# Optimization experiments

Hardware: AMD Instinct MI355X
Metric: run time of the kernel (lower is better)

The kernel has to match this reference:

```python
import jax, jax.numpy as jnp
import numpy as np
from jax import lax

B, T, U, F, K = 128, 4096, 128, 32, 31
WIN = 7  # attention_win_size
NEG = jnp.float32(-2.0**32 + 1)


def setup_inputs() -> dict:
    key = jax.random.key(0)
    ks = jax.random.split(key, 8)
    return {
        "query": jax.random.normal(ks[0], (B, U), jnp.float32),
        "state": jax.random.uniform(ks[1], (B, T), jnp.float32),
        "memory": jax.random.normal(ks[2], (B, T, U), jnp.float32) * 0.1,
        "conv_w": jax.random.normal(ks[3], (K, 1, F), jnp.float32) * 0.1,
        "conv_b": jnp.zeros((F,), jnp.float32),
        "loc_w": jax.random.normal(ks[4], (F, U), jnp.float32) * 0.1,
        "v_a": jax.random.normal(ks[5], (U,), jnp.float32) * 0.1,
        "b_a": jnp.zeros((U,), jnp.float32),
        "prev_max_attentions": jax.random.randint(ks[6], (B,), 0, T, jnp.int32),
    }


def reference(query, state, memory, conv_w, conv_b, loc_w, v_a, b_a, prev_max_attentions):
    # processed_query: [B, 1, U]
    processed_query = query[:, None, :]
    # location features: Conv1D 'same' over [B, T, 1] -> [B, T, F]
    loc_feat = lax.conv_general_dilated(
        state[:, :, None], conv_w, window_strides=(1,), padding="SAME",
        dimension_numbers=("NWC", "WIO", "NWC")) + conv_b
    # processed_location_features: [B, T, U]
    proc_loc = jnp.einsum("btf,fu->btu", loc_feat, loc_w)
    # Bahdanau location-sensitive score -> energy [B, T]
    energy = jnp.sum(v_a * jnp.tanh(memory + processed_query + proc_loc + b_a), axis=2)
    # synthesis constraint, 'window' type
    Tx = energy.shape[-1]
    idx = jnp.arange(Tx)
    key_masks = idx[None, :] < (prev_max_attentions - (WIN // 2 + (WIN % 2 != 0)))[:, None]
    reverse_masks = (idx[None, :] < (Tx - WIN // 2 - prev_max_attentions)[:, None])[:, ::-1]
    masks = key_masks | reverse_masks
    energy = jnp.where(masks, NEG, energy)
    alignments = jax.nn.softmax(energy, axis=-1)
    max_attentions = jnp.argmax(alignments, axis=-1).astype(jnp.int32)
    next_state = alignments + state  # cumulate_weights=True
    return alignments, next_state, max_attentions
```

## Files before the change

### kernel.cpp

```cpp
#include <hip/hip_runtime.h>
#include <math.h>

namespace {

constexpr int B_ = 128;
constexpr int T_ = 4096;
constexpr int U_ = 128;
constexpr int F_ = 32;
constexpr int K_ = 31;
constexpr int WIN_ = 7;
constexpr int SLICES = 4;
constexpr int SLICE_W = T_ / SLICES;
constexpr int NTHREADS = 256;

__global__ __launch_bounds__(NTHREADS) void lsa_kernel(
    const float* __restrict__ query,
    const float* __restrict__ state,
    const float* __restrict__ memory,
    const float* __restrict__ conv_w,
    const float* __restrict__ conv_b,
    const float* __restrict__ loc_w,
    const float* __restrict__ v_a,
    const float* __restrict__ b_a,
    const int*   __restrict__ prev,
    float* __restrict__ out_align,
    float* __restrict__ out_state,
    float* __restrict__ out_maxattn)
{
    const int b     = blockIdx.y;
    const int slice = blockIdx.x;
    const int tid   = threadIdx.x;

    const int pm = prev[b];
    const int lo = max(0, pm - 4);
    const int hi = min(T_ - 1, pm + 2);
    const int w  = hi - lo + 1;

    __shared__ float s_loc[WIN_][F_];
    __shared__ float s_energy[WIN_];
    __shared__ float s_align[WIN_];
    __shared__ float s_red[4];
    __shared__ int   s_amax;

    if (tid < w * F_) {
        const int j = tid / F_;
        const int f = tid % F_;
        const int t = lo + j;
        float acc = conv_b[f];
        #pragma unroll
        for (int k = 0; k < K_; ++k) {
            const int src = t + k - (K_ / 2);
            const float sv = (src >= 0 && src < T_) ? state[(size_t)b * T_ + src] : 0.f;
            acc += sv * conv_w[k * F_ + f];
        }
        s_loc[j][f] = acc;
    }
    __syncthreads();

    const int u    = tid & (U_ - 1);
    const int grp  = tid >> 7;
    const int wave = tid >> 6;
    const float q  = query[b * U_ + u];
    const float va = v_a[u];
    const float ba = b_a[u];

    for (int j0 = 0; j0 < WIN_; j0 += 2) {
        const int j = j0 + grp;
        float e = 0.f;
        if (j < w) {
            float pl = 0.f;
            #pragma unroll
            for (int f = 0; f < F_; ++f)
                pl += s_loc[j][f] * loc_w[f * U_ + u];
            const int t = lo + j;
            const float m = memory[((size_t)b * T_ + t) * U_ + u];
            e = va * tanhf(m + q + pl + ba);
        }
        #pragma unroll
        for (int off = 32; off > 0; off >>= 1)
            e += __shfl_down(e, off);
        if ((tid & 63) == 0) s_red[wave] = e;
        __syncthreads();
        if (tid == 0   && j0 < w)     s_energy[j0]     = s_red[0] + s_red[1];
        if (tid == 128 && j0 + 1 < w) s_energy[j0 + 1] = s_red[2] + s_red[3];
        __syncthreads();
    }

    if (tid == 0) {
        float mx = s_energy[0];
        for (int j = 1; j < w; ++j) mx = fmaxf(mx, s_energy[j]);
        float a[WIN_];
        float sum = 0.f;
        for (int j = 0; j < w; ++j) { a[j] = expf(s_energy[j] - mx); sum += a[j]; }
        for (int j = 0; j < w; ++j) { a[j] = a[j] / sum; s_align[j] = a[j]; }
        float best = -1.f; int bj = 0;
        for (int j = 0; j < w; ++j)
            if (a[j] > best) { best = a[j]; bj = j; }
        s_amax = lo + bj;
    }
    __syncthreads();

    const size_t row  = (size_t)b * T_;
    const int    base = slice * SLICE_W;
    const float4* st4 = reinterpret_cast<const float4*>(state + row + base);
    float4* oa4 = reinterpret_cast<float4*>(out_align + row + base);
    float4* os4 = reinterpret_cast<float4*>(out_state + row + base);

    {
        const int i  = tid;
        const int t0 = base + i * 4;
        const float4 sv = st4[i];
        float4 av;
        av.x = (t0 + 0 >= lo && t0 + 0 <= hi) ? s_align[t0 + 0 - lo] : 0.f;
        av.y = (t0 + 1 >= lo && t0 + 1 <= hi) ? s_align[t0 + 1 - lo] : 0.f;
        av.z = (t0 + 2 >= lo && t0 + 2 <= hi) ? s_align[t0 + 2 - lo] : 0.f;
        av.w = (t0 + 3 >= lo && t0 + 3 <= hi) ? s_align[t0 + 3 - lo] : 0.f;
        float4 ns;
        ns.x = sv.x + av.x;
        ns.y = sv.y + av.y;
        ns.z = sv.z + av.z;
        ns.w = sv.w + av.w;
        oa4[i] = av;
        os4[i] = ns;
    }

    if (slice == 0 && tid == 0)
        out_maxattn[b] = (float)s_amax;
}

}

extern "C" void kernel_launch(void* const* d_in, const int* in_sizes, int n_in,
                              void* d_out, int out_size, void* d_ws, size_t ws_size,
                              hipStream_t stream) {
    const float* query  = (const float*)d_in[0];
    const float* state  = (const float*)d_in[1];
    const float* memory = (const float*)d_in[2];
    const float* conv_w = (const float*)d_in[3];
    const float* conv_b = (const float*)d_in[4];
    const float* loc_w  = (const float*)d_in[5];
    const float* v_a    = (const float*)d_in[6];
    const float* b_a    = (const float*)d_in[7];
    const int*   prev   = (const int*)d_in[8];

    float* out = (float*)d_out;
    float* out_align   = out;
    float* out_state   = out + (size_t)B_ * T_;
    float* out_maxattn = out + (size_t)2 * B_ * T_;

    dim3 grid(SLICES, B_);
    lsa_kernel<<<grid, NTHREADS, 0, stream>>>(
        query, state, memory, conv_w, conv_b, loc_w, v_a, b_a, prev,
        out_align, out_state, out_maxattn);
}
```

Baseline: 15.01 us.

## Skip window computation in slices not touching it and vectorize energy per warp

```diff
diff --git a/kernel.cpp b/kernel.cpp
--- a/kernel.cpp
+++ b/kernel.cpp
@@ -30,6 +30,7 @@
     const int b     = blockIdx.y;
     const int slice = blockIdx.x;
     const int tid   = threadIdx.x;
+    const int base  = slice * SLICE_W;
 
     const int pm = prev[b];
     const int lo = max(0, pm - 4);
@@ -39,77 +40,83 @@
     __shared__ float s_loc[WIN_][F_];
     __shared__ float s_energy[WIN_];
     __shared__ float s_align[WIN_];
-    __shared__ float s_red[4];
     __shared__ int   s_amax;
 
-    if (tid < w * F_) {
-        const int j = tid / F_;
-        const int f = tid % F_;
-        const int t = lo + j;
-        float acc = conv_b[f];
-        #pragma unroll
-        for (int k = 0; k < K_; ++k) {
-            const int src = t + k - (K_ / 2);
-            const float sv = (src >= 0 && src < T_) ? state[(size_t)b * T_ + src] : 0.f;
-            acc += sv * conv_w[k * F_ + f];
+    const size_t row = (size_t)b * T_;
+    const float4 sv  = reinterpret_cast<const float4*>(state + row + base)[tid];
+
+    const bool has_pm     = (pm >= base) && (pm < base + SLICE_W);
+    const bool has_window = (base <= hi) && (base + SLICE_W > lo);
+
+    if (has_window || has_pm) {
+        const int j    = tid >> 5;
+        const int lane = tid & 31;
+
+        float4 mv = make_float4(0.f, 0.f, 0.f, 0.f);
+        if (j < w) {
+            const int t = lo + j;
+            mv = reinterpret_cast<const float4*>(memory + (row + t) * U_)[lane];
         }
-        s_loc[j][f] = acc;
-    }
-    __syncthreads();
+        const float4 q4  = reinterpret_cast<const float4*>(query + (size_t)b * U_)[lane];
+        const float4 va4 = reinterpret_cast<const float4*>(v_a)[lane];
+        const float4 ba4 = reinterpret_cast<const float4*>(b_a)[lane];
 
-    const int u    = tid & (U_ - 1);
-    const int grp  = tid >> 7;
-    const int wave = tid >> 6;
-    const float q  = query[b * U_ + u];
-    const float va = v_a[u];
-    const float ba = b_a[u];
+        if (tid < w * F_) {
+            const int cj = tid / F_;
+            const int f  = tid % F_;
+            const int t  = lo + cj;
+            float acc = conv_b[f];
+            #pragma unroll
+            for (int k = 0; k < K_; ++k) {
+                const int src = t + k - (K_ / 2);
+                const float svv = (src >= 0 && src < T_) ? state[row + src] : 0.f;
+                acc += svv * conv_w[k * F_ + f];
+            }
+            s_loc[cj][f] = acc;
+        }
+        __syncthreads();
 
-    for (int j0 = 0; j0 < WIN_; j0 += 2) {
-        const int j = j0 + grp;
         float e = 0.f;
         if (j < w) {
-            float pl = 0.f;
+            float4 pl = make_float4(0.f, 0.f, 0.f, 0.f);
             #pragma unroll
-            for (int f = 0; f < F_; ++f)
-                pl += s_loc[j][f] * loc_w[f * U_ + u];
-            const int t = lo + j;
-            const float m = memory[((size_t)b * T_ + t) * U_ + u];
-            e = va * tanhf(m + q + pl + ba);
+            for (int f = 0; f < F_; ++f) {
+                const float lf = s_loc[j][f];
+                const float4 lw = reinterpret_cast<const float4*>(loc_w + f * U_)[lane];
+                pl.x += lf * lw.x; pl.y += lf * lw.y;
+                pl.z += lf * lw.z; pl.w += lf * lw.w;
+            }
+            e  = va4.x * tanhf(mv.x + q4.x + pl.x + ba4.x);
+            e += va4.y * tanhf(mv.y + q4.y + pl.y + ba4.y);
+            e += va4.z * tanhf(mv.z + q4.z + pl.z + ba4.z);
+            e += va4.w * tanhf(mv.w + q4.w + pl.w + ba4.w);
         }
         #pragma unroll
-        for (int off = 32; off > 0; off >>= 1)
-            e += __shfl_down(e, off);
-        if ((tid & 63) == 0) s_red[wave] = e;
+        for (int off = 16; off > 0; off >>= 1)
+            e += __shfl_xor(e, off);
+        if (lane == 0 && j < w) s_energy[j] = e;
         __syncthreads();
-        if (tid == 0   && j0 < w)     s_energy[j0]     = s_red[0] + s_red[1];
-        if (tid == 128 && j0 + 1 < w) s_energy[j0 + 1] = s_red[2] + s_red[3];
+
+        if (tid == 0) {
+            float mx = s_energy[0];
+            for (int jj = 1; jj < w; ++jj) mx = fmaxf(mx, s_energy[jj]);
+            float a[WIN_];
+            float sum = 0.f;
+            for (int jj = 0; jj < w; ++jj) { a[jj] = expf(s_energy[jj] - mx); sum += a[jj]; }
+            const float inv = 1.f / sum;
+            float best = -1.f; int bj = 0;
+            for (int jj = 0; jj < w; ++jj) {
+                const float av = a[jj] * inv;
+                s_align[jj] = av;
+                if (av > best) { best = av; bj = jj; }
+            }
+            s_amax = lo + bj;
+        }
         __syncthreads();
     }
 
-    if (tid == 0) {
-        float mx = s_energy[0];
-        for (int j = 1; j < w; ++j) mx = fmaxf(mx, s_energy[j]);
-        float a[WIN_];
-        float sum = 0.f;
-        for (int j = 0; j < w; ++j) { a[j] = expf(s_energy[j] - mx); sum += a[j]; }
-        for (int j = 0; j < w; ++j) { a[j] = a[j] / sum; s_align[j] = a[j]; }
-        float best = -1.f; int bj = 0;
-        for (int j = 0; j < w; ++j)
-            if (a[j] > best) { best = a[j]; bj = j; }
-        s_amax = lo + bj;
-    }
-    __syncthreads();
-
-    const size_t row  = (size_t)b * T_;
-    const int    base = slice * SLICE_W;
-    const float4* st4 = reinterpret_cast<const float4*>(state + row + base);
-    float4* oa4 = reinterpret_cast<float4*>(out_align + row + base);
-    float4* os4 = reinterpret_cast<float4*>(out_state + row + base);
-
     {
-        const int i  = tid;
-        const int t0 = base + i * 4;
-        const float4 sv = st4[i];
+        const int t0 = base + tid * 4;
         float4 av;
         av.x = (t0 + 0 >= lo && t0 + 0 <= hi) ? s_align[t0 + 0 - lo] : 0.f;
         av.y = (t0 + 1 >= lo && t0 + 1 <= hi) ? s_align[t0 + 1 - lo] : 0.f;
@@ -120,11 +127,11 @@
         ns.y = sv.y + av.y;
         ns.z = sv.z + av.z;
         ns.w = sv.w + av.w;
-        oa4[i] = av;
-        os4[i] = ns;
+        reinterpret_cast<float4*>(out_align + row + base)[tid] = av;
+        reinterpret_cast<float4*>(out_state + row + base)[tid] = ns;
     }
 
-    if (slice == 0 && tid == 0)
+    if (has_pm && tid == 0)
         out_maxattn[b] = (float)s_amax;
 }
 
```

After: 13.33 us. 11.2% less time.
